# Kernel tuning notes

Measured on AMD Instinct MI355X. Metric: run time of the kernel, lower is better.

## Reference

```python
import jax, jax.numpy as jnp
import numpy as np

TOP_K = 2
N_EXPERTS = 8
N_EMBED = 1024
B, T = 4, 1024


def setup_inputs() -> dict:
    key = jax.random.key(0)
    k1, k2, k3 = jax.random.split(key, 3)
    x = jax.random.normal(k1, (B, T, N_EMBED), dtype=jnp.float32)
    wg_kernel = jax.random.normal(k2, (N_EMBED, N_EXPERTS), dtype=jnp.float32) * 0.02
    wg_bias = jnp.zeros((N_EXPERTS,), dtype=jnp.float32)
    # Experts.__call__ only uses w_c_fc: (E, C, C), stddev 0.02
    w_c_fc = jax.random.normal(k3, (N_EXPERTS, N_EMBED, N_EMBED), dtype=jnp.float32) * 0.02
    return {"x": x, "wg_kernel": wg_kernel, "wg_bias": wg_bias, "w_c_fc": w_c_fc}


def _dispatch(xb, logits, n_experts, top_k):
    # xb: (T, C), logits: (T, E)
    T, C = xb.shape
    top_k_logits, idx = jax.lax.top_k(logits, top_k)          # (T, k)
    probs = jax.nn.softmax(top_k_logits, axis=-1)             # (T, k)
    flat_idx = jnp.swapaxes(idx, 0, 1).ravel()                # (k*T,), k-major order
    one_hot = jax.nn.one_hot(flat_idx, n_experts, dtype=jnp.int32)
    pos = jnp.cumsum(one_hot, axis=0) * one_hot - 1           # running slot per expert
    pos = jnp.swapaxes(pos.reshape(top_k, T, n_experts), 0, 1).max(axis=2)  # (T, k)
    idx_tk = jnp.swapaxes(flat_idx.reshape(top_k, T), 0, 1)   # (T, k)
    cap = top_k * T
    x_rep = jnp.repeat(xb, top_k, axis=0)                     # (T*k, C), token-major
    buf = jnp.zeros((n_experts, cap, C), xb.dtype)
    buf = buf.at[idx_tk.ravel(), pos.ravel()].add(x_rep)      # scatter dispatch
    return probs, pos, idx_tk, buf


def reference(x, wg_kernel, wg_bias, w_c_fc):
    Bb, Tt, C = x.shape
    n_experts = w_c_fc.shape[0]
    logits = x @ wg_kernel + wg_bias                           # (B, T, E)
    probs, pos, idx, buf = jax.vmap(
        lambda xb, lb: _dispatch(xb, lb, n_experts, TOP_K))(x, logits)
    # buf: (B, E, cap, C). The original's reshape/swapaxes shuffle is a pure
    # permutation of the (B, cap) token axis that is exactly inverted after the
    # expert GEMM, so it is mathematically a no-op; apply the grouped GEMM directly.
    out = jnp.einsum('beti,eio->beto', buf, w_c_fc)            # per-expert matmul
    gathered = jax.vmap(lambda o, i, p: o[i, p])(out, idx, pos)  # (B, T, k, C)
    y = jnp.einsum('btkc,btk->btc', gathered, probs)
    return y, probs
```

## Files before the change

kernel.cpp:

```cpp
#include <hip/hip_runtime.h>
#include <math.h>

typedef __attribute__((ext_vector_type(8))) __bf16 bf16x8;
typedef __attribute__((ext_vector_type(4))) __bf16 bf16x4v;
typedef __attribute__((ext_vector_type(4))) float f32x4;

#define N_TOK  4096
#define C_DIM  1024
#define N_EXP  8
#define CAP    4096

#define WS_CNT    0
#define WS_PERM   32768
#define WS_XB     ((size_t)1 << 20)
#define WS_WT     (WS_XB + ((size_t)8 << 20))

#define GLD16(g, l)                                                        \
  __builtin_amdgcn_global_load_lds(                                        \
      (const __attribute__((address_space(1))) void*)(g),                  \
      (__attribute__((address_space(3))) void*)(l), 16, 0, 0)

__global__ __launch_bounds__(256)
void prep_kernel(const float* __restrict__ x, const float* __restrict__ wg,
                 const float* __restrict__ bias, const float* __restrict__ W,
                 __bf16* __restrict__ xb, float* __restrict__ probs,
                 __bf16* __restrict__ Wt, int* __restrict__ cnt,
                 int* __restrict__ perm) {
  __shared__ __align__(16) char smem[32768];
  __shared__ int lcnt[N_EXP], base[N_EXP];
  const int tid = threadIdx.x;

  if (blockIdx.x < 256) {
    float (*wgT)[C_DIM] = (float (*)[C_DIM])smem;
    if (tid < N_EXP) lcnt[tid] = 0;

#pragma unroll
    for (int i = 0; i < 8; ++i) {
      const float4 v = ((const float4*)wg)[i * 256 + tid];
      const int f = (i * 256 + tid) * 4;
      const int c = f >> 3;
      const int e = f & 7;
      wgT[e][c] = v.x; wgT[e + 1][c] = v.y; wgT[e + 2][c] = v.z; wgT[e + 3][c] = v.w;
    }
    __syncthreads();

    const int lane = tid & 63;
    const int wv   = tid >> 6;
    int re0[4], re1[4], rs0[4], rs1[4];

#pragma unroll
    for (int s = 0; s < 4; ++s) {
      const int t = blockIdx.x * 16 + wv * 4 + s;
      const float4* xrow = (const float4*)(x + (size_t)t * C_DIM);
      float acc[N_EXP];
#pragma unroll
      for (int e = 0; e < N_EXP; ++e) acc[e] = 0.f;

#pragma unroll
      for (int j = 0; j < 4; ++j) {
        const int c4 = j * 64 + lane;
        const float4 v = xrow[c4];
        bf16x4v bv = { (__bf16)v.x, (__bf16)v.y, (__bf16)v.z, (__bf16)v.w };
        *(bf16x4v*)(xb + (size_t)t * C_DIM + c4 * 4) = bv;
#pragma unroll
        for (int e = 0; e < N_EXP; ++e) {
          const float4 w = *(const float4*)&wgT[e][c4 * 4];
          acc[e] += v.x * w.x + v.y * w.y + v.z * w.z + v.w * w.w;
        }
      }

#pragma unroll
      for (int off = 32; off >= 1; off >>= 1) {
#pragma unroll
        for (int e = 0; e < N_EXP; ++e) acc[e] += __shfl_xor(acc[e], off, 64);
      }

      if (lane == 0) {
        float l[N_EXP];
#pragma unroll
        for (int e = 0; e < N_EXP; ++e) l[e] = acc[e] + bias[e];
        int e0 = 0;
#pragma unroll
        for (int e = 1; e < N_EXP; ++e) if (l[e] > l[e0]) e0 = e;
        int e1 = (e0 == 0) ? 1 : 0;
#pragma unroll
        for (int e = 0; e < N_EXP; ++e) if (e != e0 && l[e] > l[e1]) e1 = e;
        const float p0 = 1.f / (1.f + expf(l[e1] - l[e0]));
        probs[t * 2]     = p0;
        probs[t * 2 + 1] = 1.f - p0;
        re0[s] = e0; re1[s] = e1;
        rs0[s] = atomicAdd(&lcnt[e0], 1);
        rs1[s] = atomicAdd(&lcnt[e1], 1);
      }
    }
    __syncthreads();
    if (tid < N_EXP) base[tid] = atomicAdd(&cnt[tid], lcnt[tid]);
    __syncthreads();
    if (lane == 0) {
#pragma unroll
      for (int s = 0; s < 4; ++s) {
        const int t = blockIdx.x * 16 + wv * 4 + s;
        perm[re0[s] * CAP + base[re0[s]] + rs0[s]] = t * 2;
        perm[re1[s] * CAP + base[re1[s]] + rs1[s]] = t * 2 + 1;
      }
    }
  } else {
    __bf16 (*tile)[33] = (__bf16 (*)[33])smem;
    const int b  = blockIdx.x - 256;
    const int e  = b >> 10;
    const int r  = b & 1023;
    const int i0 = (r >> 5) * 32;
    const int o0 = (r & 31) * 32;
    const float* We  = W  + (size_t)e * C_DIM * C_DIM;
    __bf16*      Wte = Wt + (size_t)e * C_DIM * C_DIM;
    const int tx = tid & 31, ty = tid >> 5;
#pragma unroll
    for (int j = 0; j < 32; j += 8)
      tile[ty + j][tx] = (__bf16)We[(size_t)(i0 + ty + j) * C_DIM + o0 + tx];
    __syncthreads();
#pragma unroll
    for (int j = 0; j < 32; j += 8)
      Wte[(size_t)(o0 + ty + j) * C_DIM + i0 + tx] = tile[tx][ty + j];
  }
}

__global__ __launch_bounds__(128, 4)
void moe_gemm(const __bf16* __restrict__ xb, const __bf16* __restrict__ Wt,
              const int* __restrict__ cnt, const int* __restrict__ perm,
              __bf16* __restrict__ buf) {
  const int gid = blockIdx.x;
  const int e   = gid & 7;
  const int n0  = ((gid >> 3) & 7) * 128;
  const int m0  = (gid >> 6) * 64;
  const int count = cnt[e];
  if (m0 >= count) return;

  const int*    permE = perm + e * CAP;
  const __bf16* We    = Wt + (size_t)e * C_DIM * C_DIM;

  __shared__ char AsB[8192];
  __shared__ char BsB[16384];

  const int tid  = threadIdx.x;
  const int lane = tid & 63;
  const int wv   = tid >> 6;
  const int nw   = wv * 64;
  const int l16 = lane & 15, quad = lane >> 4;

  const int rsub  = tid >> 3;
  const int chunk = (tid & 7) ^ (rsub & 7);
  int tk[4];
#pragma unroll
  for (int q = 0; q < 4; ++q) {
    const int i = m0 + q * 16 + rsub;
    tk[q] = (i < count) ? (permE[i] >> 1) : 0;
  }
  const char* gB = (const char*)We + (size_t)(n0 + rsub) * 2048 + chunk * 16;
  char* ldsA = AsB + wv * 1024;
  char* ldsB = BsB + wv * 1024;

  f32x4 acc[4][4];
  const f32x4 zero = {0.f, 0.f, 0.f, 0.f};
#pragma unroll
  for (int mi = 0; mi < 4; ++mi)
#pragma unroll
    for (int ni = 0; ni < 4; ++ni) acc[mi][ni] = zero;

  for (int kt = 0; kt < 16; ++kt) {
    const int kb = kt * 128;
#pragma unroll
    for (int q = 0; q < 4; ++q)
      GLD16((const char*)xb + (size_t)tk[q] * 2048 + kb + chunk * 16,
            ldsA + q * 2048);
#pragma unroll
    for (int q = 0; q < 8; ++q)
      GLD16(gB + (size_t)q * 16 * 2048 + kb, ldsB + q * 2048);
    __syncthreads();

#pragma unroll
    for (int ks = 0; ks < 2; ++ks) {
      bf16x8 af[4], bfr[4];
#pragma unroll
      for (int mi = 0; mi < 4; ++mi) {
        const int rA = mi * 16 + l16;
        af[mi] = *(const bf16x8*)(AsB + rA * 128 +
                                  (((ks * 4 + quad) ^ (rA & 7)) << 4));
      }
#pragma unroll
      for (int ni = 0; ni < 4; ++ni) {
        const int rB = nw + ni * 16 + l16;
        bfr[ni] = *(const bf16x8*)(BsB + rB * 128 +
                                   (((ks * 4 + quad) ^ (rB & 7)) << 4));
      }
#pragma unroll
      for (int mi = 0; mi < 4; ++mi)
#pragma unroll
        for (int ni = 0; ni < 4; ++ni)
          acc[mi][ni] = __builtin_amdgcn_mfma_f32_16x16x32_bf16(
              af[mi], bfr[ni], acc[mi][ni], 0, 0, 0);
    }
    __syncthreads();
  }

#pragma unroll
  for (int mi = 0; mi < 4; ++mi) {
#pragma unroll
    for (int r = 0; r < 4; ++r) {
      const int i = m0 + mi * 16 + quad * 4 + r;
      if (i < count) {
        const int pe = permE[i];
        __bf16* orow = buf + (size_t)(pe >> 1) * 2048 + (pe & 1) * 1024 +
                       n0 + nw + l16;
#pragma unroll
        for (int ni = 0; ni < 4; ++ni)
          orow[ni * 16] = (__bf16)acc[mi][ni][r];
      }
    }
  }
}

__global__ __launch_bounds__(256)
void combine(const float* __restrict__ probs, float* __restrict__ y) {
  const int t = blockIdx.x;
  const int c = threadIdx.x * 4;
  const __bf16* bt = (const __bf16*)(y + (size_t)t * C_DIM);
  const bf16x4v b0 = *(const bf16x4v*)(bt + c);
  const bf16x4v b1 = *(const bf16x4v*)(bt + 1024 + c);
  const float p0 = probs[2 * t], p1 = probs[2 * t + 1];
  __syncthreads();
  float4 o = { p0 * (float)b0[0] + p1 * (float)b1[0],
               p0 * (float)b0[1] + p1 * (float)b1[1],
               p0 * (float)b0[2] + p1 * (float)b1[2],
               p0 * (float)b0[3] + p1 * (float)b1[3] };
  *(float4*)(y + (size_t)t * C_DIM + c) = o;
}

extern "C" void kernel_launch(void* const* d_in, const int* in_sizes, int n_in,
                              void* d_out, int out_size, void* d_ws, size_t ws_size,
                              hipStream_t stream) {
  const float* x    = (const float*)d_in[0];
  const float* wg   = (const float*)d_in[1];
  const float* bias = (const float*)d_in[2];
  const float* wcfc = (const float*)d_in[3];

  float* y     = (float*)d_out;
  float* probs = y + (size_t)N_TOK * C_DIM;
  __bf16* buf  = (__bf16*)d_out;

  char* ws   = (char*)d_ws;
  int*    cnt  = (int*)(ws + WS_CNT);
  int*    perm = (int*)(ws + WS_PERM);
  __bf16* xb   = (__bf16*)(ws + WS_XB);
  __bf16* Wt   = (__bf16*)(ws + WS_WT);

  hipMemsetAsync(cnt, 0, N_EXP * sizeof(int), stream);

  prep_kernel<<<256 + 8192, 256, 0, stream>>>(x, wg, bias, wcfc, xb, probs,
                                              Wt, cnt, perm);
  moe_gemm<<<8 * 8 * 64, 128, 0, stream>>>(xb, Wt, cnt, perm, buf);
  combine<<<N_TOK, 256, 0, stream>>>(probs, y);
}
```

Before: 147.4 us.

## Use 128x128 GEMM tiles with split-K into two partial buffers

The expert GEMM now uses 256-thread blocks computing 128x128 output tiles (2x2 waves) instead of 64x128 tiles. The K dimension is split in half across two block groups, each writing bf16 partials to separate workspace buffers. The combine kernel sums the two partials before applying the routing weights. This raises data reuse per block and keeps the grid populated despite the larger tiles. The cost is extra partial-buffer traffic and an additional bf16 rounding of each half-sum.

```diff
diff --git a/kernel.cpp b/kernel.cpp
--- a/kernel.cpp
+++ b/kernel.cpp
@@ -14,6 +14,8 @@
 #define WS_PERM   32768
 #define WS_XB     ((size_t)1 << 20)
 #define WS_WT     (WS_XB + ((size_t)8 << 20))
+#define WS_P0     (WS_WT + ((size_t)16 << 20))
+#define WS_P1     (WS_P0 + ((size_t)16 << 20))
 
 #define GLD16(g, l)                                                        \
   __builtin_amdgcn_global_load_lds(                                        \
@@ -124,38 +126,42 @@
   }
 }
 
-__global__ __launch_bounds__(128, 4)
+__global__ __launch_bounds__(256)
 void moe_gemm(const __bf16* __restrict__ xb, const __bf16* __restrict__ Wt,
               const int* __restrict__ cnt, const int* __restrict__ perm,
-              __bf16* __restrict__ buf) {
+              __bf16* __restrict__ P0, __bf16* __restrict__ P1) {
   const int gid = blockIdx.x;
   const int e   = gid & 7;
   const int n0  = ((gid >> 3) & 7) * 128;
-  const int m0  = (gid >> 6) * 64;
+  const int kh  = (gid >> 6) & 1;
+  const int m0  = (gid >> 7) * 128;
   const int count = cnt[e];
   if (m0 >= count) return;
+  __bf16* buf = kh ? P1 : P0;
 
   const int*    permE = perm + e * CAP;
   const __bf16* We    = Wt + (size_t)e * C_DIM * C_DIM;
 
-  __shared__ char AsB[8192];
+  __shared__ char AsB[16384];
   __shared__ char BsB[16384];
 
   const int tid  = threadIdx.x;
   const int lane = tid & 63;
   const int wv   = tid >> 6;
-  const int nw   = wv * 64;
+  const int wr = wv >> 1, wc = wv & 1;
+  const int mw = wr * 64, nw = wc * 64;
   const int l16 = lane & 15, quad = lane >> 4;
 
   const int rsub  = tid >> 3;
   const int chunk = (tid & 7) ^ (rsub & 7);
+  const int khb   = kh * 1024;
   int tk[4];
 #pragma unroll
   for (int q = 0; q < 4; ++q) {
-    const int i = m0 + q * 16 + rsub;
+    const int i = m0 + q * 32 + rsub;
     tk[q] = (i < count) ? (permE[i] >> 1) : 0;
   }
-  const char* gB = (const char*)We + (size_t)(n0 + rsub) * 2048 + chunk * 16;
+  const char* gB = (const char*)We + (size_t)(n0 + rsub) * 2048 + khb + chunk * 16;
   char* ldsA = AsB + wv * 1024;
   char* ldsB = BsB + wv * 1024;
 
@@ -166,15 +172,15 @@
 #pragma unroll
     for (int ni = 0; ni < 4; ++ni) acc[mi][ni] = zero;
 
-  for (int kt = 0; kt < 16; ++kt) {
+  for (int kt = 0; kt < 8; ++kt) {
     const int kb = kt * 128;
 #pragma unroll
     for (int q = 0; q < 4; ++q)
-      GLD16((const char*)xb + (size_t)tk[q] * 2048 + kb + chunk * 16,
-            ldsA + q * 2048);
-#pragma unroll
-    for (int q = 0; q < 8; ++q)
-      GLD16(gB + (size_t)q * 16 * 2048 + kb, ldsB + q * 2048);
+      GLD16((const char*)xb + (size_t)tk[q] * 2048 + khb + kb + chunk * 16,
+            ldsA + q * 4096);
+#pragma unroll
+    for (int q = 0; q < 4; ++q)
+      GLD16(gB + (size_t)q * 32 * 2048 + kb, ldsB + q * 4096);
     __syncthreads();
 
 #pragma unroll
@@ -182,7 +188,7 @@
       bf16x8 af[4], bfr[4];
 #pragma unroll
       for (int mi = 0; mi < 4; ++mi) {
-        const int rA = mi * 16 + l16;
+        const int rA = mw + mi * 16 + l16;
         af[mi] = *(const bf16x8*)(AsB + rA * 128 +
                                   (((ks * 4 + quad) ^ (rA & 7)) << 4));
       }
@@ -206,7 +212,7 @@
   for (int mi = 0; mi < 4; ++mi) {
 #pragma unroll
     for (int r = 0; r < 4; ++r) {
-      const int i = m0 + mi * 16 + quad * 4 + r;
+      const int i = m0 + mw + mi * 16 + quad * 4 + r;
       if (i < count) {
         const int pe = permE[i];
         __bf16* orow = buf + (size_t)(pe >> 1) * 2048 + (pe & 1) * 1024 +
@@ -220,18 +226,20 @@
 }
 
 __global__ __launch_bounds__(256)
-void combine(const float* __restrict__ probs, float* __restrict__ y) {
+void combine(const __bf16* __restrict__ P0, const __bf16* __restrict__ P1,
+             const float* __restrict__ probs, float* __restrict__ y) {
   const int t = blockIdx.x;
   const int c = threadIdx.x * 4;
-  const __bf16* bt = (const __bf16*)(y + (size_t)t * C_DIM);
-  const bf16x4v b0 = *(const bf16x4v*)(bt + c);
-  const bf16x4v b1 = *(const bf16x4v*)(bt + 1024 + c);
+  const bf16x4v a0 = *(const bf16x4v*)(P0 + (size_t)t * 2048 + c);
+  const bf16x4v a1 = *(const bf16x4v*)(P0 + (size_t)t * 2048 + 1024 + c);
+  const bf16x4v b0 = *(const bf16x4v*)(P1 + (size_t)t * 2048 + c);
+  const bf16x4v b1 = *(const bf16x4v*)(P1 + (size_t)t * 2048 + 1024 + c);
   const float p0 = probs[2 * t], p1 = probs[2 * t + 1];
-  __syncthreads();
-  float4 o = { p0 * (float)b0[0] + p1 * (float)b1[0],
-               p0 * (float)b0[1] + p1 * (float)b1[1],
-               p0 * (float)b0[2] + p1 * (float)b1[2],
-               p0 * (float)b0[3] + p1 * (float)b1[3] };
+  float4 o;
+#pragma unroll
+  for (int j = 0; j < 4; ++j)
+    ((float*)&o)[j] = p0 * ((float)a0[j] + (float)b0[j]) +
+                      p1 * ((float)a1[j] + (float)b1[j]);
   *(float4*)(y + (size_t)t * C_DIM + c) = o;
 }
 
@@ -245,18 +253,19 @@
 
   float* y     = (float*)d_out;
   float* probs = y + (size_t)N_TOK * C_DIM;
-  __bf16* buf  = (__bf16*)d_out;
 
   char* ws   = (char*)d_ws;
   int*    cnt  = (int*)(ws + WS_CNT);
   int*    perm = (int*)(ws + WS_PERM);
   __bf16* xb   = (__bf16*)(ws + WS_XB);
   __bf16* Wt   = (__bf16*)(ws + WS_WT);
+  __bf16* P0   = (__bf16*)(ws + WS_P0);
+  __bf16* P1   = (__bf16*)(ws + WS_P1);
 
   hipMemsetAsync(cnt, 0, N_EXP * sizeof(int), stream);
 
   prep_kernel<<<256 + 8192, 256, 0, stream>>>(x, wg, bias, wcfc, xb, probs,
                                               Wt, cnt, perm);
-  moe_gemm<<<8 * 8 * 64, 128, 0, stream>>>(xb, Wt, cnt, perm, buf);
-  combine<<<N_TOK, 256, 0, stream>>>(probs, y);
-}
+  moe_gemm<<<8 * 8 * 2 * 32, 256, 0, stream>>>(xb, Wt, cnt, perm, P0, P1);
+  combine<<<N_TOK, 256, 0, stream>>>(P0, P1, probs, y);
+}
```

Result: faster. 139.5 us (-5.4%).

## Drop LDS staging in MoE GEMM, load fragments directly with register double-buffering

Applied to the files above, without the earlier changes.

The expert GEMM no longer stages A/B tiles through shared memory with global_load_lds and barriers. Each wave now loads its MFMA fragments straight from global memory into registers, double-buffered across k-steps. The block tile also grows to 128x128 with 4 waves in a 2x2 layout. This removes LDS traffic and the syncthreads, but gives up cross-wave data sharing, so each wave issues redundant, poorly coalesced 16-byte global loads that rely on L2/L1 for reuse.

```diff
diff --git a/kernel.cpp b/kernel.cpp
--- a/kernel.cpp
+++ b/kernel.cpp
@@ -14,11 +14,6 @@
 #define WS_PERM   32768
 #define WS_XB     ((size_t)1 << 20)
 #define WS_WT     (WS_XB + ((size_t)8 << 20))
-
-#define GLD16(g, l)                                                        \
-  __builtin_amdgcn_global_load_lds(                                        \
-      (const __attribute__((address_space(1))) void*)(g),                  \
-      (__attribute__((address_space(3))) void*)(l), 16, 0, 0)
 
 __global__ __launch_bounds__(256)
 void prep_kernel(const float* __restrict__ x, const float* __restrict__ wg,
@@ -124,40 +119,40 @@
   }
 }
 
-__global__ __launch_bounds__(128, 4)
+__global__ __launch_bounds__(256)
 void moe_gemm(const __bf16* __restrict__ xb, const __bf16* __restrict__ Wt,
               const int* __restrict__ cnt, const int* __restrict__ perm,
               __bf16* __restrict__ buf) {
   const int gid = blockIdx.x;
   const int e   = gid & 7;
   const int n0  = ((gid >> 3) & 7) * 128;
-  const int m0  = (gid >> 6) * 64;
+  const int m0  = (gid >> 6) * 128;
   const int count = cnt[e];
   if (m0 >= count) return;
 
   const int*    permE = perm + e * CAP;
   const __bf16* We    = Wt + (size_t)e * C_DIM * C_DIM;
-
-  __shared__ char AsB[8192];
-  __shared__ char BsB[16384];
 
   const int tid  = threadIdx.x;
   const int lane = tid & 63;
   const int wv   = tid >> 6;
-  const int nw   = wv * 64;
+  const int wr = wv >> 1, wc = wv & 1;
+  const int mw = wr * 64, nw = wc * 64;
   const int l16 = lane & 15, quad = lane >> 4;
 
-  const int rsub  = tid >> 3;
-  const int chunk = (tid & 7) ^ (rsub & 7);
-  int tk[4];
-#pragma unroll
-  for (int q = 0; q < 4; ++q) {
-    const int i = m0 + q * 16 + rsub;
-    tk[q] = (i < count) ? (permE[i] >> 1) : 0;
-  }
-  const char* gB = (const char*)We + (size_t)(n0 + rsub) * 2048 + chunk * 16;
-  char* ldsA = AsB + wv * 1024;
-  char* ldsB = BsB + wv * 1024;
+  const char* Arow[4];
+  const char* Brow[4];
+#pragma unroll
+  for (int mi = 0; mi < 4; ++mi) {
+    const int i = m0 + mw + mi * 16 + l16;
+    const int tok = (i < count) ? (permE[i] >> 1) : 0;
+    Arow[mi] = (const char*)xb + (size_t)tok * 2048;
+  }
+#pragma unroll
+  for (int ni = 0; ni < 4; ++ni)
+    Brow[ni] = (const char*)We + (size_t)(n0 + nw + ni * 16 + l16) * 2048;
+
+  const int qb = quad * 16;
 
   f32x4 acc[4][4];
   const f32x4 zero = {0.f, 0.f, 0.f, 0.f};
@@ -166,47 +161,47 @@
 #pragma unroll
     for (int ni = 0; ni < 4; ++ni) acc[mi][ni] = zero;
 
-  for (int kt = 0; kt < 16; ++kt) {
-    const int kb = kt * 128;
-#pragma unroll
-    for (int q = 0; q < 4; ++q)
-      GLD16((const char*)xb + (size_t)tk[q] * 2048 + kb + chunk * 16,
-            ldsA + q * 2048);
-#pragma unroll
-    for (int q = 0; q < 8; ++q)
-      GLD16(gB + (size_t)q * 16 * 2048 + kb, ldsB + q * 2048);
-    __syncthreads();
-
-#pragma unroll
-    for (int ks = 0; ks < 2; ++ks) {
-      bf16x8 af[4], bfr[4];
-#pragma unroll
-      for (int mi = 0; mi < 4; ++mi) {
-        const int rA = mi * 16 + l16;
-        af[mi] = *(const bf16x8*)(AsB + rA * 128 +
-                                  (((ks * 4 + quad) ^ (rA & 7)) << 4));
-      }
-#pragma unroll
-      for (int ni = 0; ni < 4; ++ni) {
-        const int rB = nw + ni * 16 + l16;
-        bfr[ni] = *(const bf16x8*)(BsB + rB * 128 +
-                                   (((ks * 4 + quad) ^ (rB & 7)) << 4));
-      }
-#pragma unroll
-      for (int mi = 0; mi < 4; ++mi)
-#pragma unroll
-        for (int ni = 0; ni < 4; ++ni)
-          acc[mi][ni] = __builtin_amdgcn_mfma_f32_16x16x32_bf16(
-              af[mi], bfr[ni], acc[mi][ni], 0, 0, 0);
-    }
-    __syncthreads();
+  bf16x8 aP[2][4], bP[2][4];
+#pragma unroll
+  for (int mi = 0; mi < 4; ++mi) aP[0][mi] = *(const bf16x8*)(Arow[mi] + qb);
+#pragma unroll
+  for (int ni = 0; ni < 4; ++ni) bP[0][ni] = *(const bf16x8*)(Brow[ni] + qb);
+
+  for (int s = 0; s < 32; s += 2) {
+    const int kb1 = (s + 1) * 64 + qb;
+    if (s + 1 < 32) {
+#pragma unroll
+      for (int mi = 0; mi < 4; ++mi) aP[1][mi] = *(const bf16x8*)(Arow[mi] + kb1);
+#pragma unroll
+      for (int ni = 0; ni < 4; ++ni) bP[1][ni] = *(const bf16x8*)(Brow[ni] + kb1);
+    }
+#pragma unroll
+    for (int mi = 0; mi < 4; ++mi)
+#pragma unroll
+      for (int ni = 0; ni < 4; ++ni)
+        acc[mi][ni] = __builtin_amdgcn_mfma_f32_16x16x32_bf16(
+            aP[0][mi], bP[0][ni], acc[mi][ni], 0, 0, 0);
+
+    const int kb2 = (s + 2) * 64 + qb;
+    if (s + 2 < 32) {
+#pragma unroll
+      for (int mi = 0; mi < 4; ++mi) aP[0][mi] = *(const bf16x8*)(Arow[mi] + kb2);
+#pragma unroll
+      for (int ni = 0; ni < 4; ++ni) bP[0][ni] = *(const bf16x8*)(Brow[ni] + kb2);
+    }
+#pragma unroll
+    for (int mi = 0; mi < 4; ++mi)
+#pragma unroll
+      for (int ni = 0; ni < 4; ++ni)
+        acc[mi][ni] = __builtin_amdgcn_mfma_f32_16x16x32_bf16(
+            aP[1][mi], bP[1][ni], acc[mi][ni], 0, 0, 0);
   }
 
 #pragma unroll
   for (int mi = 0; mi < 4; ++mi) {
 #pragma unroll
     for (int r = 0; r < 4; ++r) {
-      const int i = m0 + mi * 16 + quad * 4 + r;
+      const int i = m0 + mw + mi * 16 + quad * 4 + r;
       if (i < count) {
         const int pe = permE[i];
         __bf16* orow = buf + (size_t)(pe >> 1) * 2048 + (pe & 1) * 1024 +
@@ -257,6 +252,6 @@
 
   prep_kernel<<<256 + 8192, 256, 0, stream>>>(x, wg, bias, wcfc, xb, probs,
                                               Wt, cnt, perm);
-  moe_gemm<<<8 * 8 * 64, 128, 0, stream>>>(xb, Wt, cnt, perm, buf);
+  moe_gemm<<<8 * 8 * 32, 256, 0, stream>>>(xb, Wt, cnt, perm, buf);
   combine<<<N_TOK, 256, 0, stream>>>(probs, y);
 }
```

Result: slower. 191.4 us (+29.9%).

## Enlarge MoE GEMM tile to 128x128 with 4 waves and double-buffered LDS

Applied to the files above, without the earlier changes.

The expert GEMM now uses 256-thread blocks with a 2x2 wave layout covering a 128x128 output tile instead of 64x128, halving the grid. The single LDS buffer becomes a double buffer, so the next K-slice's async global-to-LDS loads are issued before computing on the current slice, with one barrier per iteration. This aims to hide load latency and raise reuse of each loaded tile, at the cost of more LDS per block (64KB), possibly lower occupancy, and more padding waste for experts whose token counts are not multiples of 128.

```diff
diff --git a/kernel.cpp b/kernel.cpp
--- a/kernel.cpp
+++ b/kernel.cpp
@@ -124,27 +124,28 @@
   }
 }
 
-__global__ __launch_bounds__(128, 4)
+__global__ __launch_bounds__(256)
 void moe_gemm(const __bf16* __restrict__ xb, const __bf16* __restrict__ Wt,
               const int* __restrict__ cnt, const int* __restrict__ perm,
               __bf16* __restrict__ buf) {
   const int gid = blockIdx.x;
   const int e   = gid & 7;
   const int n0  = ((gid >> 3) & 7) * 128;
-  const int m0  = (gid >> 6) * 64;
+  const int m0  = (gid >> 6) * 128;
   const int count = cnt[e];
   if (m0 >= count) return;
 
   const int*    permE = perm + e * CAP;
   const __bf16* We    = Wt + (size_t)e * C_DIM * C_DIM;
 
-  __shared__ char AsB[8192];
-  __shared__ char BsB[16384];
+  __shared__ char AsB[2][16384];
+  __shared__ char BsB[2][16384];
 
   const int tid  = threadIdx.x;
   const int lane = tid & 63;
   const int wv   = tid >> 6;
-  const int nw   = wv * 64;
+  const int wr = wv >> 1, wc = wv & 1;
+  const int mw = wr * 64, nw = wc * 64;
   const int l16 = lane & 15, quad = lane >> 4;
 
   const int rsub  = tid >> 3;
@@ -152,12 +153,22 @@
   int tk[4];
 #pragma unroll
   for (int q = 0; q < 4; ++q) {
-    const int i = m0 + q * 16 + rsub;
+    const int i = m0 + q * 32 + rsub;
     tk[q] = (i < count) ? (permE[i] >> 1) : 0;
   }
   const char* gB = (const char*)We + (size_t)(n0 + rsub) * 2048 + chunk * 16;
-  char* ldsA = AsB + wv * 1024;
-  char* ldsB = BsB + wv * 1024;
+
+#define STAGE(pb, kbyte)                                                     \
+  {                                                                          \
+    _Pragma("unroll")                                                        \
+    for (int q = 0; q < 4; ++q)                                              \
+      GLD16((const char*)xb + (size_t)tk[q] * 2048 + (kbyte) + chunk * 16,   \
+            AsB[pb] + wv * 1024 + q * 4096);                                 \
+    _Pragma("unroll")                                                        \
+    for (int q = 0; q < 4; ++q)                                              \
+      GLD16(gB + (size_t)q * 32 * 2048 + (kbyte),                            \
+            BsB[pb] + wv * 1024 + q * 4096);                                 \
+  }
 
   f32x4 acc[4][4];
   const f32x4 zero = {0.f, 0.f, 0.f, 0.f};
@@ -166,30 +177,28 @@
 #pragma unroll
     for (int ni = 0; ni < 4; ++ni) acc[mi][ni] = zero;
 
+  STAGE(0, 0);
+
   for (int kt = 0; kt < 16; ++kt) {
-    const int kb = kt * 128;
-#pragma unroll
-    for (int q = 0; q < 4; ++q)
-      GLD16((const char*)xb + (size_t)tk[q] * 2048 + kb + chunk * 16,
-            ldsA + q * 2048);
-#pragma unroll
-    for (int q = 0; q < 8; ++q)
-      GLD16(gB + (size_t)q * 16 * 2048 + kb, ldsB + q * 2048);
-    __syncthreads();
-
+    const int cur = kt & 1;
+    __syncthreads();
+    if (kt < 15) STAGE(cur ^ 1, (kt + 1) * 128);
+
+    const char* Ab = AsB[cur];
+    const char* Bb = BsB[cur];
 #pragma unroll
     for (int ks = 0; ks < 2; ++ks) {
       bf16x8 af[4], bfr[4];
 #pragma unroll
       for (int mi = 0; mi < 4; ++mi) {
-        const int rA = mi * 16 + l16;
-        af[mi] = *(const bf16x8*)(AsB + rA * 128 +
+        const int rA = mw + mi * 16 + l16;
+        af[mi] = *(const bf16x8*)(Ab + rA * 128 +
                                   (((ks * 4 + quad) ^ (rA & 7)) << 4));
       }
 #pragma unroll
       for (int ni = 0; ni < 4; ++ni) {
         const int rB = nw + ni * 16 + l16;
-        bfr[ni] = *(const bf16x8*)(BsB + rB * 128 +
+        bfr[ni] = *(const bf16x8*)(Bb + rB * 128 +
                                    (((ks * 4 + quad) ^ (rB & 7)) << 4));
       }
 #pragma unroll
@@ -199,14 +208,13 @@
           acc[mi][ni] = __builtin_amdgcn_mfma_f32_16x16x32_bf16(
               af[mi], bfr[ni], acc[mi][ni], 0, 0, 0);
     }
-    __syncthreads();
   }
 
 #pragma unroll
   for (int mi = 0; mi < 4; ++mi) {
 #pragma unroll
     for (int r = 0; r < 4; ++r) {
-      const int i = m0 + mi * 16 + quad * 4 + r;
+      const int i = m0 + mw + mi * 16 + quad * 4 + r;
       if (i < count) {
         const int pe = permE[i];
         __bf16* orow = buf + (size_t)(pe >> 1) * 2048 + (pe & 1) * 1024 +
@@ -257,6 +265,6 @@
 
   prep_kernel<<<256 + 8192, 256, 0, stream>>>(x, wg, bias, wcfc, xb, probs,
                                               Wt, cnt, perm);
-  moe_gemm<<<8 * 8 * 64, 128, 0, stream>>>(xb, Wt, cnt, perm, buf);
+  moe_gemm<<<8 * 8 * 32, 256, 0, stream>>>(xb, Wt, cnt, perm, buf);
   combine<<<N_TOK, 256, 0, stream>>>(probs, y);
 }
```

After: 159.1 us. 1.08x slower.
